# Performance work log

Hardware: AMD Instinct MI355X
Metric: run time of the kernel (lower is better)

Reference implementation:

```python
import jax, jax.numpy as jnp
import numpy as np

B, N, K = 8, 2048, 16
C_IN, HID, C_OUT = 128, 128, 128
MSG_DIM = 2 * C_IN + 3


def setup_inputs() -> dict:
    key = jax.random.key(0)
    ks = jax.random.split(key, 9)
    h = jax.random.normal(ks[0], (B, N, C_IN), dtype=jnp.float32)
    pos = jax.random.normal(ks[1], (B, N, 3), dtype=jnp.float32)
    idx = jax.random.randint(ks[2], (B, N, K), 0, N, dtype=jnp.int64)
    # MLP params (Linear: y = x @ W.T + b; store as (in, out) for einsum-free matmul)
    s1 = 1.0 / np.sqrt(MSG_DIM)
    s2 = 1.0 / np.sqrt(HID)
    W1 = jax.random.uniform(ks[3], (MSG_DIM, HID), minval=-s1, maxval=s1, dtype=jnp.float32)
    b1 = jax.random.uniform(ks[4], (HID,), minval=-s1, maxval=s1, dtype=jnp.float32)
    W2 = jax.random.uniform(ks[5], (HID, C_OUT), minval=-s2, maxval=s2, dtype=jnp.float32)
    b2 = jax.random.uniform(ks[6], (C_OUT,), minval=-s2, maxval=s2, dtype=jnp.float32)
    gamma = jnp.ones((C_OUT,), dtype=jnp.float32)
    beta = jnp.zeros((C_OUT,), dtype=jnp.float32)
    return {"h": h, "pos": pos, "idx": idx, "W1": W1, "b1": b1,
            "W2": W2, "b2": b2, "gamma": gamma, "beta": beta}


def _gather(feats, idx):
    # feats: (B,N,C), idx: (B,N,k) -> (B,N,k,C)
    return jax.vmap(lambda f, i: f[i])(feats, idx)


def _layernorm(x, gamma, beta, eps=1e-5):
    mu = jnp.mean(x, axis=-1, keepdims=True)
    var = jnp.mean(jnp.square(x - mu), axis=-1, keepdims=True)
    return (x - mu) * jax.lax.rsqrt(var + eps) * gamma + beta


def reference(h, pos, idx, W1, b1, W2, b2, gamma, beta):
    # h: (B,N,C), pos: (B,N,3), idx: (B,N,k)
    h_j = _gather(h, idx)                      # (B,N,k,C)
    rel = _gather(pos, idx) - pos[:, :, None]  # (B,N,k,3)
    h_i = jnp.broadcast_to(h[:, :, None, :], h_j.shape)
    msg = jnp.concatenate([h_i, h_j - h_i, rel], axis=-1)   # (B,N,k,2C+3)
    x = jax.nn.gelu(msg @ W1 + b1, approximate=False)       # (B,N,k,H)
    x = jax.nn.gelu(x @ W2 + b2, approximate=False)         # (B,N,k,O)
    out = jnp.max(x, axis=2)                                 # (B,N,O)
    return _layernorm(out, gamma, beta)
```

## Files before the change

kernel.cpp:

```cpp
#include <hip/hip_runtime.h>
#include <math.h>

#define NPTS 2048
#define KNBR 16

typedef __attribute__((ext_vector_type(8))) short bf16x8;
typedef __attribute__((ext_vector_type(4))) float f32x4;
union U8 { bf16x8 v; unsigned u[4]; };

static __device__ __forceinline__ unsigned pk2(float lo, float hi) {
    unsigned r;
    asm("v_cvt_pk_bf16_f32 %0, %1, %2" : "=v"(r) : "v"(lo), "v"(hi));
    return r;
}

static __device__ __forceinline__ float gelu(float x) {
    float x2 = x * x;
    float u  = x * fmaf(x2, 0.044715f, 1.0f);
    float e  = __expf(u * -1.5957691216057308f);
    return x * __builtin_amdgcn_rcpf(1.0f + e);
}

#define HSTR 136
#define LDS_SHORTS (36864 + 16 * 16 * HSTR)

__global__ __launch_bounds__(1024, 4) void edgeconv_fused(
    const float* __restrict__ h, const float* __restrict__ pos,
    const int* __restrict__ idx,
    const float* __restrict__ W1, const float* __restrict__ W2,
    const float* __restrict__ b1, const float* __restrict__ b2,
    const float* __restrict__ gamma, const float* __restrict__ beta,
    float* __restrict__ out)
{
    extern __shared__ short lds[];
    const int tid = threadIdx.x, wave = tid >> 6, lane = tid & 63;
    const int quad = lane >> 4, lm = lane & 15;

    for (int c = tid; c < 6656; c += 1024) {
        const int l = c & 63, fi = c >> 6;
        const int lrow = (l >> 4) * 8, lcol = l & 15;
        U8 t;
        if (fi < 40) {
            int ks = fi % 5, nt = fi / 5;
            int row0 = 128 + ks * 32 + lrow, col = nt * 16 + lcol;
            #pragma unroll
            for (int p = 0; p < 4; ++p) {
                int r0 = row0 + 2 * p;
                float v0 = (r0     < 259) ? W1[r0 * 128 + col]       : 0.f;
                float v1 = (r0 + 1 < 259) ? W1[(r0 + 1) * 128 + col] : 0.f;
                t.u[p] = pk2(v0, v1);
            }
        } else if (fi < 72) {
            int f2 = fi - 40, ks = f2 & 3, nt = f2 >> 2;
            int row0 = ks * 32 + lrow, col = nt * 16 + lcol;
            #pragma unroll
            for (int p = 0; p < 4; ++p)
                t.u[p] = pk2(W2[(row0 + 2*p) * 128 + col],
                             W2[(row0 + 2*p + 1) * 128 + col]);
        } else {
            int f2 = fi - 72, ks = f2 & 3, nt = f2 >> 2;
            int row0 = ks * 32 + lrow, col = nt * 16 + lcol;
            #pragma unroll
            for (int p = 0; p < 4; ++p)
                t.u[p] = pk2(W1[(row0 + 2*p) * 128 + col],
                             W1[(row0 + 2*p + 1) * 128 + col]);
        }
        ((bf16x8*)lds)[c] = t.v;
    }

    float b1v[8], b2v[8];
    #pragma unroll
    for (int nt = 0; nt < 8; ++nt) {
        b1v[nt] = b1[nt * 16 + lm];
        b2v[nt] = b2[nt * 16 + lm];
    }
    const float gv0 = gamma[(quad * 2) * 16 + lm];
    const float gv1 = gamma[(quad * 2 + 1) * 16 + lm];
    const float be0 = beta[(quad * 2) * 16 + lm];
    const float be1 = beta[(quad * 2 + 1) * 16 + lm];

    __syncthreads();

    const bf16x8* w1frag  = (const bf16x8*)lds;
    const bf16x8* w2frag  = (const bf16x8*)lds + 2560;
    const bf16x8* w1afrag = (const bf16x8*)lds + 4608;
    short* hrow = lds + 36864 + wave * 16 * HSTR;

    const int sb = (blockIdx.x & 7) * 32 + (blockIdx.x >> 3);
    const int node0 = sb * 64 + wave * 4;

    f32x4 basev[8];
    #pragma unroll
    for (int nt = 0; nt < 8; ++nt)
        basev[nt] = (f32x4){b1v[nt], b1v[nt], b1v[nt], b1v[nt]};
    {
        const float4* hsrc = (const float4*)h + (size_t)(node0 + (lm & 3)) * 32;
        bf16x8 af[4];
        #pragma unroll
        for (int ks = 0; ks < 4; ++ks) {
            float4 p0 = hsrc[ks * 8 + quad * 2];
            float4 p1 = hsrc[ks * 8 + quad * 2 + 1];
            U8 t;
            t.u[0] = pk2(p0.x, p0.y); t.u[1] = pk2(p0.z, p0.w);
            t.u[2] = pk2(p1.x, p1.y); t.u[3] = pk2(p1.z, p1.w);
            af[ks] = t.v;
        }
        #pragma unroll
        for (int ks = 0; ks < 4; ++ks)
            #pragma unroll
            for (int nt = 0; nt < 8; ++nt)
                basev[nt] = __builtin_amdgcn_mfma_f32_16x16x32_bf16(
                    af[ks], w1afrag[(nt * 4 + ks) * 64 + lane], basev[nt], 0, 0, 0);
    }
    __syncthreads();

    #pragma unroll
    for (int ni = 0; ni < 4; ++ni) {
        const int node = node0 + ni;
        const int b = node >> 11, n = node & 2047;
        const float4* hb4 = (const float4*)h + (size_t)b * NPTS * 32;
        const float*  pb  = pos + (size_t)b * NPTS * 3;

        const int jm = idx[node * KNBR + lm];

        bf16x8 afrag[4];
        #pragma unroll
        for (int ks = 0; ks < 4; ++ks) {
            float4 a0 = hb4[n  * 32 + ks * 8 + quad * 2];
            float4 a1 = hb4[n  * 32 + ks * 8 + quad * 2 + 1];
            float4 j0 = hb4[jm * 32 + ks * 8 + quad * 2];
            float4 j1 = hb4[jm * 32 + ks * 8 + quad * 2 + 1];
            U8 t;
            t.u[0] = pk2(j0.x - a0.x, j0.y - a0.y);
            t.u[1] = pk2(j0.z - a0.z, j0.w - a0.w);
            t.u[2] = pk2(j1.x - a1.x, j1.y - a1.y);
            t.u[3] = pk2(j1.z - a1.z, j1.w - a1.w);
            afrag[ks] = t.v;
        }
        U8 rt; rt.u[0] = 0; rt.u[1] = 0; rt.u[2] = 0; rt.u[3] = 0;
        if (quad == 0) {
            float rx = pb[3 * jm]     - pb[3 * n];
            float ry = pb[3 * jm + 1] - pb[3 * n + 1];
            float rz = pb[3 * jm + 2] - pb[3 * n + 2];
            rt.u[0] = pk2(rx, ry);
            rt.u[1] = pk2(rz, 0.0f);
        }

        f32x4 acc[8];
        #pragma unroll
        for (int nt = 0; nt < 8; ++nt) {
            float bv = basev[nt][ni];
            acc[nt] = (f32x4){bv, bv, bv, bv};
        }
        #pragma unroll
        for (int ks = 0; ks < 4; ++ks)
            #pragma unroll
            for (int nt = 0; nt < 8; ++nt)
                acc[nt] = __builtin_amdgcn_mfma_f32_16x16x32_bf16(
                    afrag[ks], w1frag[(nt * 5 + ks) * 64 + lane], acc[nt], 0, 0, 0);
        #pragma unroll
        for (int nt = 0; nt < 8; ++nt)
            acc[nt] = __builtin_amdgcn_mfma_f32_16x16x32_bf16(
                rt.v, w1frag[(nt * 5 + 4) * 64 + lane], acc[nt], 0, 0, 0);

        #pragma unroll
        for (int nt = 0; nt < 8; ++nt)
            #pragma unroll
            for (int r = 0; r < 4; ++r) {
                float g = gelu(acc[nt][r]);
                hrow[(quad * 4 + r) * HSTR + nt * 16 + lm] = (short)pk2(g, g);
            }
        asm volatile("s_waitcnt lgkmcnt(0)" ::: "memory");

        bf16x8 a2[4];
        #pragma unroll
        for (int ks = 0; ks < 4; ++ks)
            a2[ks] = *(const bf16x8*)(hrow + lm * HSTR + ks * 32 + quad * 8);

        f32x4 acc2[8];
        #pragma unroll
        for (int nt = 0; nt < 8; ++nt) acc2[nt] = (f32x4){0.f, 0.f, 0.f, 0.f};
        #pragma unroll
        for (int ks = 0; ks < 4; ++ks)
            #pragma unroll
            for (int nt = 0; nt < 8; ++nt)
                acc2[nt] = __builtin_amdgcn_mfma_f32_16x16x32_bf16(
                    a2[ks], w2frag[(nt * 4 + ks) * 64 + lane], acc2[nt], 0, 0, 0);

        float v[8];
        #pragma unroll
        for (int nt = 0; nt < 8; ++nt) {
            float mx = fmaxf(fmaxf(acc2[nt][0], acc2[nt][1]),
                             fmaxf(acc2[nt][2], acc2[nt][3]));
            float mn = fminf(fminf(acc2[nt][0], acc2[nt][1]),
                             fminf(acc2[nt][2], acc2[nt][3]));
            mx = fmaxf(mx, __shfl_xor(mx, 16, 64));
            mx = fmaxf(mx, __shfl_xor(mx, 32, 64));
            mn = fminf(mn, __shfl_xor(mn, 16, 64));
            mn = fminf(mn, __shfl_xor(mn, 32, 64));
            mx += b2v[nt]; mn += b2v[nt];
            v[nt] = fmaxf(gelu(mx), gelu(mn));
        }

        float s = 0.f, s2 = 0.f;
        #pragma unroll
        for (int nt = 0; nt < 8; ++nt) { s += v[nt]; s2 += v[nt] * v[nt]; }
        #pragma unroll
        for (int off = 1; off <= 8; off <<= 1) {
            s  += __shfl_xor(s,  off, 64);
            s2 += __shfl_xor(s2, off, 64);
        }
        const float mu  = s * (1.0f / 128.0f);
        const float var = s2 * (1.0f / 128.0f) - mu * mu;
        const float inv = rsqrtf(var + 1e-5f);

        float* orow = out + (size_t)node * 128;
        orow[(quad * 2) * 16 + lm]     = (v[quad * 2]     - mu) * inv * gv0 + be0;
        orow[(quad * 2 + 1) * 16 + lm] = (v[quad * 2 + 1] - mu) * inv * gv1 + be1;
    }
}

extern "C" void kernel_launch(void* const* d_in, const int* in_sizes, int n_in,
                              void* d_out, int out_size, void* d_ws, size_t ws_size,
                              hipStream_t stream) {
    const float* h     = (const float*)d_in[0];
    const float* pos   = (const float*)d_in[1];
    const int*   idx   = (const int*)  d_in[2];
    const float* W1    = (const float*)d_in[3];
    const float* b1    = (const float*)d_in[4];
    const float* W2    = (const float*)d_in[5];
    const float* b2    = (const float*)d_in[6];
    const float* gamma = (const float*)d_in[7];
    const float* beta  = (const float*)d_in[8];
    float* out = (float*)d_out;

    hipFuncSetAttribute((const void*)edgeconv_fused,
                        hipFuncAttributeMaxDynamicSharedMemorySize,
                        LDS_SHORTS * 2);
    edgeconv_fused<<<256, 1024, LDS_SHORTS * 2, stream>>>(
        h, pos, idx, W1, W2, b1, b2, gamma, beta, out);
}
```

Measured before the change: 122.4 us.

## Process node pairs with prefetched neighbor gathers and chunked GELU staging

Each wave now handles two nodes at a time, sharing each W1/W2 fragment LDS load across two MFMA chains. Neighbor feature and position gathers for the next pair are issued early into registers so global latency overlaps compute. The per-node first-layer base is written to LDS instead of kept in registers, and the GELU staging buffer is cut to 32-column chunks. This raises register pressure and adds extra LDS waits per chunk, and LDS grows to 144 KB.

```diff
diff --git a/kernel.cpp b/kernel.cpp
--- a/kernel.cpp
+++ b/kernel.cpp
@@ -1,5 +1,4 @@
 #include <hip/hip_runtime.h>
-#include <math.h>
 
 #define NPTS 2048
 #define KNBR 16
@@ -21,8 +20,8 @@
     return x * __builtin_amdgcn_rcpf(1.0f + e);
 }
 
-#define HSTR 136
-#define LDS_SHORTS (36864 + 16 * 16 * HSTR)
+#define STG 40
+#define LDS_BYTES 147456
 
 __global__ __launch_bounds__(1024, 4) void edgeconv_fused(
     const float* __restrict__ h, const float* __restrict__ pos,
@@ -33,6 +32,7 @@
     float* __restrict__ out)
 {
     extern __shared__ short lds[];
+    float* ldsF = (float*)lds;
     const int tid = threadIdx.x, wave = tid >> 6, lane = tid & 63;
     const int quad = lane >> 4, lm = lane & 15;
 
@@ -84,17 +84,26 @@
     const bf16x8* w1frag  = (const bf16x8*)lds;
     const bf16x8* w2frag  = (const bf16x8*)lds + 2560;
     const bf16x8* w1afrag = (const bf16x8*)lds + 4608;
-    short* hrow = lds + 36864 + wave * 16 * HSTR;
+    short* stg   = lds  + 36864 + wave * 1280;
+    float* baseF = ldsF + 28672 + wave * 512;
 
     const int sb = (blockIdx.x & 7) * 32 + (blockIdx.x >> 3);
     const int node0 = sb * 64 + wave * 4;
-
-    f32x4 basev[8];
+    const int bidx = node0 >> 11;
+    const float4* hb4 = (const float4*)h + (size_t)bidx * NPTS * 32;
+    const float*  pb  = pos + (size_t)bidx * NPTS * 3;
+    const int nloc = node0 & 2047;
+
+    int idxv[4];
     #pragma unroll
-    for (int nt = 0; nt < 8; ++nt)
-        basev[nt] = (f32x4){b1v[nt], b1v[nt], b1v[nt], b1v[nt]};
+    for (int ni = 0; ni < 4; ++ni)
+        idxv[ni] = idx[(node0 + ni) * KNBR + lm];
+
+    float4 hjA[8], hjB[8];
+    float pjxA, pjyA, pjzA, pjxB, pjyB, pjzB;
+
     {
-        const float4* hsrc = (const float4*)h + (size_t)(node0 + (lm & 3)) * 32;
+        const float4* hsrc = hb4 + (size_t)(nloc + (lm & 3)) * 32;
         bf16x8 af[4];
         #pragma unroll
         for (int ks = 0; ks < 4; ++ks) {
@@ -105,118 +114,173 @@
             t.u[2] = pk2(p1.x, p1.y); t.u[3] = pk2(p1.z, p1.w);
             af[ks] = t.v;
         }
+        f32x4 bacc[8];
+        #pragma unroll
+        for (int nt = 0; nt < 8; ++nt)
+            bacc[nt] = (f32x4){b1v[nt], b1v[nt], b1v[nt], b1v[nt]};
         #pragma unroll
         for (int ks = 0; ks < 4; ++ks)
             #pragma unroll
             for (int nt = 0; nt < 8; ++nt)
-                basev[nt] = __builtin_amdgcn_mfma_f32_16x16x32_bf16(
-                    af[ks], w1afrag[(nt * 4 + ks) * 64 + lane], basev[nt], 0, 0, 0);
+                bacc[nt] = __builtin_amdgcn_mfma_f32_16x16x32_bf16(
+                    af[ks], w1afrag[(nt * 4 + ks) * 64 + lane], bacc[nt], 0, 0, 0);
+
+        {
+            const float4* ja = hb4 + (size_t)idxv[0] * 32;
+            const float4* jb = hb4 + (size_t)idxv[1] * 32;
+            #pragma unroll
+            for (int ks = 0; ks < 4; ++ks) {
+                hjA[2*ks]   = ja[ks * 8 + quad * 2];
+                hjA[2*ks+1] = ja[ks * 8 + quad * 2 + 1];
+                hjB[2*ks]   = jb[ks * 8 + quad * 2];
+                hjB[2*ks+1] = jb[ks * 8 + quad * 2 + 1];
+            }
+            pjxA = pb[3*idxv[0]]; pjyA = pb[3*idxv[0]+1]; pjzA = pb[3*idxv[0]+2];
+            pjxB = pb[3*idxv[1]]; pjyB = pb[3*idxv[1]+1]; pjzB = pb[3*idxv[1]+2];
+        }
+
+        if (quad == 0)
+            #pragma unroll
+            for (int nt = 0; nt < 8; ++nt)
+                #pragma unroll
+                for (int r = 0; r < 4; ++r)
+                    baseF[r * 128 + nt * 16 + lm] = bacc[nt][r];
     }
     __syncthreads();
 
     #pragma unroll
-    for (int ni = 0; ni < 4; ++ni) {
-        const int node = node0 + ni;
-        const int b = node >> 11, n = node & 2047;
-        const float4* hb4 = (const float4*)h + (size_t)b * NPTS * 32;
-        const float*  pb  = pos + (size_t)b * NPTS * 3;
-
-        const int jm = idx[node * KNBR + lm];
-
-        bf16x8 afrag[4];
-        #pragma unroll
-        for (int ks = 0; ks < 4; ++ks) {
-            float4 a0 = hb4[n  * 32 + ks * 8 + quad * 2];
-            float4 a1 = hb4[n  * 32 + ks * 8 + quad * 2 + 1];
-            float4 j0 = hb4[jm * 32 + ks * 8 + quad * 2];
-            float4 j1 = hb4[jm * 32 + ks * 8 + quad * 2 + 1];
-            U8 t;
-            t.u[0] = pk2(j0.x - a0.x, j0.y - a0.y);
-            t.u[1] = pk2(j0.z - a0.z, j0.w - a0.w);
-            t.u[2] = pk2(j1.x - a1.x, j1.y - a1.y);
-            t.u[3] = pk2(j1.z - a1.z, j1.w - a1.w);
-            afrag[ks] = t.v;
-        }
-        U8 rt; rt.u[0] = 0; rt.u[1] = 0; rt.u[2] = 0; rt.u[3] = 0;
-        if (quad == 0) {
-            float rx = pb[3 * jm]     - pb[3 * n];
-            float ry = pb[3 * jm + 1] - pb[3 * n + 1];
-            float rz = pb[3 * jm + 2] - pb[3 * n + 2];
-            rt.u[0] = pk2(rx, ry);
-            rt.u[1] = pk2(rz, 0.0f);
-        }
-
-        f32x4 acc[8];
+    for (int pr = 0; pr < 2; ++pr) {
+        const int na = pr * 2, nb = pr * 2 + 1;
+
+        bf16x8 afA[4], afB[4];
+        U8 rlA, rlB;
+        {
+            const float4* hiA4 = hb4 + (size_t)(nloc + na) * 32;
+            const float4* hiB4 = hb4 + (size_t)(nloc + nb) * 32;
+            #pragma unroll
+            for (int ks = 0; ks < 4; ++ks) {
+                float4 a0 = hiA4[ks * 8 + quad * 2];
+                float4 a1 = hiA4[ks * 8 + quad * 2 + 1];
+                float4 b0 = hiB4[ks * 8 + quad * 2];
+                float4 b1_ = hiB4[ks * 8 + quad * 2 + 1];
+                float4 j0 = hjA[2*ks], j1 = hjA[2*ks+1];
+                float4 k0 = hjB[2*ks], k1 = hjB[2*ks+1];
+                U8 t;
+                t.u[0] = pk2(j0.x - a0.x, j0.y - a0.y);
+                t.u[1] = pk2(j0.z - a0.z, j0.w - a0.w);
+                t.u[2] = pk2(j1.x - a1.x, j1.y - a1.y);
+                t.u[3] = pk2(j1.z - a1.z, j1.w - a1.w);
+                afA[ks] = t.v;
+                t.u[0] = pk2(k0.x - b0.x, k0.y - b0.y);
+                t.u[1] = pk2(k0.z - b0.z, k0.w - b0.w);
+                t.u[2] = pk2(k1.x - b1_.x, k1.y - b1_.y);
+                t.u[3] = pk2(k1.z - b1_.z, k1.w - b1_.w);
+                afB[ks] = t.v;
+            }
+            rlA.u[0] = 0; rlA.u[1] = 0; rlA.u[2] = 0; rlA.u[3] = 0;
+            rlB.u[0] = 0; rlB.u[1] = 0; rlB.u[2] = 0; rlB.u[3] = 0;
+            if (quad == 0) {
+                int ia = nloc + na, ib = nloc + nb;
+                rlA.u[0] = pk2(pjxA - pb[3*ia], pjyA - pb[3*ia+1]);
+                rlA.u[1] = pk2(pjzA - pb[3*ia+2], 0.f);
+                rlB.u[0] = pk2(pjxB - pb[3*ib], pjyB - pb[3*ib+1]);
+                rlB.u[1] = pk2(pjzB - pb[3*ib+2], 0.f);
+            }
+        }
+
+        bf16x8 a2A[4], a2B[4];
+        #pragma unroll
+        for (int ks2 = 0; ks2 < 4; ++ks2) {
+            #pragma unroll
+            for (int ntl = 0; ntl < 2; ++ntl) {
+                const int nt = ks2 * 2 + ntl;
+                float bA = baseF[na * 128 + nt * 16 + lm];
+                float bB = baseF[nb * 128 + nt * 16 + lm];
+                f32x4 cA = (f32x4){bA, bA, bA, bA};
+                f32x4 cB = (f32x4){bB, bB, bB, bB};
+                #pragma unroll
+                for (int ks = 0; ks < 4; ++ks) {
+                    bf16x8 w = w1frag[(nt * 5 + ks) * 64 + lane];
+                    cA = __builtin_amdgcn_mfma_f32_16x16x32_bf16(afA[ks], w, cA, 0, 0, 0);
+                    cB = __builtin_amdgcn_mfma_f32_16x16x32_bf16(afB[ks], w, cB, 0, 0, 0);
+                }
+                {
+                    bf16x8 w = w1frag[(nt * 5 + 4) * 64 + lane];
+                    cA = __builtin_amdgcn_mfma_f32_16x16x32_bf16(rlA.v, w, cA, 0, 0, 0);
+                    cB = __builtin_amdgcn_mfma_f32_16x16x32_bf16(rlB.v, w, cB, 0, 0, 0);
+                }
+                #pragma unroll
+                for (int r = 0; r < 4; ++r) {
+                    float gA = gelu(cA[r]), gB = gelu(cB[r]);
+                    stg[      (quad * 4 + r) * STG + ntl * 16 + lm] = (short)pk2(gA, gA);
+                    stg[640 + (quad * 4 + r) * STG + ntl * 16 + lm] = (short)pk2(gB, gB);
+                }
+            }
+            asm volatile("s_waitcnt lgkmcnt(0)" ::: "memory");
+            a2A[ks2] = *(const bf16x8*)(stg +       lm * STG + quad * 8);
+            a2B[ks2] = *(const bf16x8*)(stg + 640 + lm * STG + quad * 8);
+            asm volatile("s_waitcnt lgkmcnt(0)" ::: "memory");
+        }
+
+        if (pr == 0) {
+            const float4* ja = hb4 + (size_t)idxv[2] * 32;
+            const float4* jb = hb4 + (size_t)idxv[3] * 32;
+            #pragma unroll
+            for (int ks = 0; ks < 4; ++ks) {
+                hjA[2*ks]   = ja[ks * 8 + quad * 2];
+                hjA[2*ks+1] = ja[ks * 8 + quad * 2 + 1];
+                hjB[2*ks]   = jb[ks * 8 + quad * 2];
+                hjB[2*ks+1] = jb[ks * 8 + quad * 2 + 1];
+            }
+            pjxA = pb[3*idxv[2]]; pjyA = pb[3*idxv[2]+1]; pjzA = pb[3*idxv[2]+2];
+            pjxB = pb[3*idxv[3]]; pjyB = pb[3*idxv[3]+1]; pjzB = pb[3*idxv[3]+2];
+        }
+
+        float vA[8], vB[8];
         #pragma unroll
         for (int nt = 0; nt < 8; ++nt) {
-            float bv = basev[nt][ni];
-            acc[nt] = (f32x4){bv, bv, bv, bv};
-        }
-        #pragma unroll
-        for (int ks = 0; ks < 4; ++ks)
-            #pragma unroll
-            for (int nt = 0; nt < 8; ++nt)
-                acc[nt] = __builtin_amdgcn_mfma_f32_16x16x32_bf16(
-                    afrag[ks], w1frag[(nt * 5 + ks) * 64 + lane], acc[nt], 0, 0, 0);
-        #pragma unroll
-        for (int nt = 0; nt < 8; ++nt)
-            acc[nt] = __builtin_amdgcn_mfma_f32_16x16x32_bf16(
-                rt.v, w1frag[(nt * 5 + 4) * 64 + lane], acc[nt], 0, 0, 0);
-
-        #pragma unroll
-        for (int nt = 0; nt < 8; ++nt)
-            #pragma unroll
-            for (int r = 0; r < 4; ++r) {
-                float g = gelu(acc[nt][r]);
-                hrow[(quad * 4 + r) * HSTR + nt * 16 + lm] = (short)pk2(g, g);
-            }
-        asm volatile("s_waitcnt lgkmcnt(0)" ::: "memory");
-
-        bf16x8 a2[4];
-        #pragma unroll
-        for (int ks = 0; ks < 4; ++ks)
-            a2[ks] = *(const bf16x8*)(hrow + lm * HSTR + ks * 32 + quad * 8);
-
-        f32x4 acc2[8];
-        #pragma unroll
-        for (int nt = 0; nt < 8; ++nt) acc2[nt] = (f32x4){0.f, 0.f, 0.f, 0.f};
-        #pragma unroll
-        for (int ks = 0; ks < 4; ++ks)
-            #pragma unroll
-            for (int nt = 0; nt < 8; ++nt)
-                acc2[nt] = __builtin_amdgcn_mfma_f32_16x16x32_bf16(
-                    a2[ks], w2frag[(nt * 4 + ks) * 64 + lane], acc2[nt], 0, 0, 0);
-
-        float v[8];
-        #pragma unroll
-        for (int nt = 0; nt < 8; ++nt) {
-            float mx = fmaxf(fmaxf(acc2[nt][0], acc2[nt][1]),
-                             fmaxf(acc2[nt][2], acc2[nt][3]));
-            float mn = fminf(fminf(acc2[nt][0], acc2[nt][1]),
-                             fminf(acc2[nt][2], acc2[nt][3]));
-            mx = fmaxf(mx, __shfl_xor(mx, 16, 64));
-            mx = fmaxf(mx, __shfl_xor(mx, 32, 64));
-            mn = fminf(mn, __shfl_xor(mn, 16, 64));
-            mn = fminf(mn, __shfl_xor(mn, 32, 64));
-            mx += b2v[nt]; mn += b2v[nt];
-            v[nt] = fmaxf(gelu(mx), gelu(mn));
-        }
-
-        float s = 0.f, s2 = 0.f;
-        #pragma unroll
-        for (int nt = 0; nt < 8; ++nt) { s += v[nt]; s2 += v[nt] * v[nt]; }
-        #pragma unroll
-        for (int off = 1; off <= 8; off <<= 1) {
-            s  += __shfl_xor(s,  off, 64);
-            s2 += __shfl_xor(s2, off, 64);
-        }
-        const float mu  = s * (1.0f / 128.0f);
-        const float var = s2 * (1.0f / 128.0f) - mu * mu;
-        const float inv = rsqrtf(var + 1e-5f);
-
-        float* orow = out + (size_t)node * 128;
-        orow[(quad * 2) * 16 + lm]     = (v[quad * 2]     - mu) * inv * gv0 + be0;
-        orow[(quad * 2 + 1) * 16 + lm] = (v[quad * 2 + 1] - mu) * inv * gv1 + be1;
+            f32x4 cA = (f32x4){0.f, 0.f, 0.f, 0.f};
+            f32x4 cB = (f32x4){0.f, 0.f, 0.f, 0.f};
+            #pragma unroll
+            for (int ks = 0; ks < 4; ++ks) {
+                bf16x8 w = w2frag[(nt * 4 + ks) * 64 + lane];
+                cA = __builtin_amdgcn_mfma_f32_16x16x32_bf16(a2A[ks], w, cA, 0, 0, 0);
+                cB = __builtin_amdgcn_mfma_f32_16x16x32_bf16(a2B[ks], w, cB, 0, 0, 0);
+            }
+            float mxA = fmaxf(fmaxf(cA[0], cA[1]), fmaxf(cA[2], cA[3]));
+            float mnA = fminf(fminf(cA[0], cA[1]), fminf(cA[2], cA[3]));
+            float mxB = fmaxf(fmaxf(cB[0], cB[1]), fmaxf(cB[2], cB[3]));
+            float mnB = fminf(fminf(cB[0], cB[1]), fminf(cB[2], cB[3]));
+            mxA = fmaxf(mxA, __shfl_xor(mxA, 16, 64));
+            mxA = fmaxf(mxA, __shfl_xor(mxA, 32, 64));
+            mnA = fminf(mnA, __shfl_xor(mnA, 16, 64));
+            mnA = fminf(mnA, __shfl_xor(mnA, 32, 64));
+            mxB = fmaxf(mxB, __shfl_xor(mxB, 16, 64));
+            mxB = fmaxf(mxB, __shfl_xor(mxB, 32, 64));
+            mnB = fminf(mnB, __shfl_xor(mnB, 16, 64));
+            mnB = fminf(mnB, __shfl_xor(mnB, 32, 64));
+            vA[nt] = fmaxf(gelu(mxA + b2v[nt]), gelu(mnA + b2v[nt]));
+            vB[nt] = fmaxf(gelu(mxB + b2v[nt]), gelu(mnB + b2v[nt]));
+        }
+
+        #pragma unroll
+        for (int u = 0; u < 2; ++u) {
+            const float* v = u ? vB : vA;
+            float s = 0.f, s2 = 0.f;
+            #pragma unroll
+            for (int nt = 0; nt < 8; ++nt) { s += v[nt]; s2 += v[nt] * v[nt]; }
+            #pragma unroll
+            for (int off = 1; off <= 8; off <<= 1) {
+                s  += __shfl_xor(s,  off, 64);
+                s2 += __shfl_xor(s2, off, 64);
+            }
+            const float mu  = s * (1.0f / 128.0f);
+            const float var = s2 * (1.0f / 128.0f) - mu * mu;
+            const float inv = rsqrtf(var + 1e-5f);
+            float* orow = out + (size_t)(node0 + pr * 2 + u) * 128;
+            orow[(quad * 2) * 16 + lm]     = (v[quad * 2]     - mu) * inv * gv0 + be0;
+            orow[(quad * 2 + 1) * 16 + lm] = (v[quad * 2 + 1] - mu) * inv * gv1 + be1;
+        }
     }
 }
 
@@ -235,8 +299,7 @@
     float* out = (float*)d_out;
 
     hipFuncSetAttribute((const void*)edgeconv_fused,
-                        hipFuncAttributeMaxDynamicSharedMemorySize,
-                        LDS_SHORTS * 2);
-    edgeconv_fused<<<256, 1024, LDS_SHORTS * 2, stream>>>(
+                        hipFuncAttributeMaxDynamicSharedMemorySize, LDS_BYTES);
+    edgeconv_fused<<<256, 1024, LDS_BYTES, stream>>>(
         h, pos, idx, W1, W2, b1, b2, gamma, beta, out);
 }
```

After: 123.4 us. No clear change (+0.8%).

## Precompute per-node W1 projection and gather projected features instead of raw h

Applied to the files above, without the earlier changes.

The first linear layer is split algebraically: h_i@(W1a-W1b) plus b1 is computed once per center node, and h_j@W1b is precomputed for every node by a new first kernel into a bf16 workspace. The edge kernel then gathers these 128-wide bf16 rows, adds the relative-position term with scalar FMAs, and applies GELU. This removes the per-edge first-layer MFMAs and the LDS round-trip for the hidden activations. The cost is an extra kernel launch, a global write and re-read of the projected table, and bf16 rounding of the precomputed projection. It also prefetches the next node's gathered rows and switches GELU to exp2.

```diff
diff --git a/kernel.cpp b/kernel.cpp
--- a/kernel.cpp
+++ b/kernel.cpp
@@ -1,5 +1,4 @@
 #include <hip/hip_runtime.h>
-#include <math.h>
 
 #define NPTS 2048
 #define KNBR 16
@@ -7,6 +6,7 @@
 typedef __attribute__((ext_vector_type(8))) short bf16x8;
 typedef __attribute__((ext_vector_type(4))) float f32x4;
 union U8 { bf16x8 v; unsigned u[4]; };
+union F4 { f32x4 v; float4 q; };
 
 static __device__ __forceinline__ unsigned pk2(float lo, float hi) {
     unsigned r;
@@ -17,63 +17,116 @@
 static __device__ __forceinline__ float gelu(float x) {
     float x2 = x * x;
     float u  = x * fmaf(x2, 0.044715f, 1.0f);
-    float e  = __expf(u * -1.5957691216057308f);
+    float e  = __builtin_amdgcn_exp2f(u * -2.3022083f);
     return x * __builtin_amdgcn_rcpf(1.0f + e);
 }
 
-#define HSTR 136
-#define LDS_SHORTS (36864 + 16 * 16 * HSTR)
-
-__global__ __launch_bounds__(1024, 4) void edgeconv_fused(
+__global__ __launch_bounds__(1024) void edge_phase1(
+    const float* __restrict__ h, const float* __restrict__ W1,
+    short* __restrict__ G)
+{
+    __shared__ short w1bfs[16384];
+    const int tid = threadIdx.x, lane = tid & 63, wave = tid >> 6;
+    const int quad = lane >> 4, lm = lane & 15;
+
+    for (int c = tid; c < 2048; c += 1024) {
+        const int l = c & 63, fi = c >> 6;
+        const int lrow = (l >> 4) * 8, lcol = l & 15;
+        const int ks = fi & 3, nt = fi >> 2;
+        const int row0 = 128 + ks * 32 + lrow, col = nt * 16 + lcol;
+        U8 t;
+        #pragma unroll
+        for (int p = 0; p < 4; ++p)
+            t.u[p] = pk2(W1[(row0 + 2*p) * 128 + col],
+                         W1[(row0 + 2*p + 1) * 128 + col]);
+        ((bf16x8*)w1bfs)[c] = t.v;
+    }
+    __syncthreads();
+    const bf16x8* w1bf = (const bf16x8*)w1bfs;
+
+    const int sb = (blockIdx.x & 7) * 32 + (blockIdx.x >> 3);
+    const int node0 = sb * 64 + wave * 4;
+    const int bidx = node0 >> 11, nloc = node0 & 2047;
+    const float4* hb4 = (const float4*)h + (size_t)bidx * NPTS * 32;
+    short* Gb = G + (size_t)bidx * NPTS * 128;
+
+    const float4* hsrc = hb4 + (size_t)(nloc + (lm & 3)) * 32;
+    bf16x8 af[4];
+    #pragma unroll
+    for (int ks = 0; ks < 4; ++ks) {
+        float4 p0 = hsrc[ks * 8 + quad * 2];
+        float4 p1 = hsrc[ks * 8 + quad * 2 + 1];
+        U8 t;
+        t.u[0] = pk2(p0.x, p0.y); t.u[1] = pk2(p0.z, p0.w);
+        t.u[2] = pk2(p1.x, p1.y); t.u[3] = pk2(p1.z, p1.w);
+        af[ks] = t.v;
+    }
+    f32x4 gacc[8];
+    #pragma unroll
+    for (int nt = 0; nt < 8; ++nt) gacc[nt] = (f32x4){0.f, 0.f, 0.f, 0.f};
+    #pragma unroll
+    for (int ks = 0; ks < 4; ++ks)
+        #pragma unroll
+        for (int nt = 0; nt < 8; ++nt)
+            gacc[nt] = __builtin_amdgcn_mfma_f32_16x16x32_bf16(
+                w1bf[(nt * 4 + ks) * 64 + lane], af[ks], gacc[nt], 0, 0, 0);
+
+    if (lm < 4)
+        #pragma unroll
+        for (int nt = 0; nt < 8; ++nt) {
+            uint2 gw;
+            gw.x = pk2(gacc[nt][0], gacc[nt][1]);
+            gw.y = pk2(gacc[nt][2], gacc[nt][3]);
+            *(uint2*)(Gb + (size_t)(nloc + lm) * 128 + nt * 16 + quad * 4) = gw;
+        }
+}
+
+#define LDS2_BYTES 99840
+
+__global__ __launch_bounds__(1024, 4) void edge_phase2(
     const float* __restrict__ h, const float* __restrict__ pos,
     const int* __restrict__ idx,
     const float* __restrict__ W1, const float* __restrict__ W2,
     const float* __restrict__ b1, const float* __restrict__ b2,
     const float* __restrict__ gamma, const float* __restrict__ beta,
+    const short* __restrict__ G,
     float* __restrict__ out)
 {
     extern __shared__ short lds[];
+    float* ldsF = (float*)lds;
     const int tid = threadIdx.x, wave = tid >> 6, lane = tid & 63;
     const int quad = lane >> 4, lm = lane & 15;
 
-    for (int c = tid; c < 6656; c += 1024) {
+    for (int c = tid; c < 4096; c += 1024) {
         const int l = c & 63, fi = c >> 6;
         const int lrow = (l >> 4) * 8, lcol = l & 15;
         U8 t;
-        if (fi < 40) {
-            int ks = fi % 5, nt = fi / 5;
-            int row0 = 128 + ks * 32 + lrow, col = nt * 16 + lcol;
-            #pragma unroll
-            for (int p = 0; p < 4; ++p) {
-                int r0 = row0 + 2 * p;
-                float v0 = (r0     < 259) ? W1[r0 * 128 + col]       : 0.f;
-                float v1 = (r0 + 1 < 259) ? W1[(r0 + 1) * 128 + col] : 0.f;
-                t.u[p] = pk2(v0, v1);
-            }
-        } else if (fi < 72) {
-            int f2 = fi - 40, ks = f2 & 3, nt = f2 >> 2;
+        if (fi < 32) {
+            int ks = fi & 3, nt = fi >> 2;
             int row0 = ks * 32 + lrow, col = nt * 16 + lcol;
             #pragma unroll
             for (int p = 0; p < 4; ++p)
                 t.u[p] = pk2(W2[(row0 + 2*p) * 128 + col],
                              W2[(row0 + 2*p + 1) * 128 + col]);
         } else {
-            int f2 = fi - 72, ks = f2 & 3, nt = f2 >> 2;
+            int f2 = fi - 32, ks = f2 & 3, nt = f2 >> 2;
             int row0 = ks * 32 + lrow, col = nt * 16 + lcol;
             #pragma unroll
-            for (int p = 0; p < 4; ++p)
-                t.u[p] = pk2(W1[(row0 + 2*p) * 128 + col],
-                             W1[(row0 + 2*p + 1) * 128 + col]);
+            for (int p = 0; p < 4; ++p) {
+                int r0 = row0 + 2 * p;
+                float v0 = W1[r0 * 128 + col]       - W1[(r0 + 128) * 128 + col];
+                float v1 = W1[(r0 + 1) * 128 + col] - W1[(r0 + 129) * 128 + col];
+                t.u[p] = pk2(v0, v1);
+            }
         }
         ((bf16x8*)lds)[c] = t.v;
     }
-
-    float b1v[8], b2v[8];
-    #pragma unroll
-    for (int nt = 0; nt < 8; ++nt) {
-        b1v[nt] = b1[nt * 16 + lm];
-        b2v[nt] = b2[nt * 16 + lm];
-    }
+    if (tid < 384)
+        ldsF[16384 + tid] = W1[(256 + (tid >> 7)) * 128 + (tid & 127)];
+
+    float b2v[8];
+    #pragma unroll
+    for (int nt = 0; nt < 8; ++nt) b2v[nt] = b2[nt * 16 + lm];
     const float gv0 = gamma[(quad * 2) * 16 + lm];
     const float gv1 = gamma[(quad * 2 + 1) * 16 + lm];
     const float be0 = beta[(quad * 2) * 16 + lm];
@@ -81,20 +134,30 @@
 
     __syncthreads();
 
-    const bf16x8* w1frag  = (const bf16x8*)lds;
-    const bf16x8* w2frag  = (const bf16x8*)lds + 2560;
-    const bf16x8* w1afrag = (const bf16x8*)lds + 4608;
-    short* hrow = lds + 36864 + wave * 16 * HSTR;
+    const bf16x8* w2frag = (const bf16x8*)lds;
+    const bf16x8* w1df   = (const bf16x8*)lds + 2048;
+    const float*  w1rL   = ldsF + 16384;
+    float* baseW = ldsF + 16768 + wave * 512;
 
     const int sb = (blockIdx.x & 7) * 32 + (blockIdx.x >> 3);
     const int node0 = sb * 64 + wave * 4;
-
-    f32x4 basev[8];
-    #pragma unroll
-    for (int nt = 0; nt < 8; ++nt)
-        basev[nt] = (f32x4){b1v[nt], b1v[nt], b1v[nt], b1v[nt]};
+    const int bidx = node0 >> 11, nloc = node0 & 2047;
+    const float4* hb4 = (const float4*)h + (size_t)bidx * NPTS * 32;
+    const float*  pb  = pos + (size_t)bidx * NPTS * 3;
+    const short*  Gb  = G + (size_t)bidx * NPTS * 128;
+
+    int idxv[4];
+    #pragma unroll
+    for (int ni = 0; ni < 4; ++ni)
+        idxv[ni] = idx[(node0 + ni) * KNBR + lm];
+
+    bf16x8 gcur[4], gnxt[4];
+    #pragma unroll
+    for (int ks = 0; ks < 4; ++ks)
+        gcur[ks] = *(const bf16x8*)(Gb + (size_t)idxv[0] * 128 + ks * 32 + quad * 8);
+
     {
-        const float4* hsrc = (const float4*)h + (size_t)(node0 + (lm & 3)) * 32;
+        const float4* hsrc = hb4 + (size_t)(nloc + (lm & 3)) * 32;
         bf16x8 af[4];
         #pragma unroll
         for (int ks = 0; ks < 4; ++ks) {
@@ -105,106 +168,95 @@
             t.u[2] = pk2(p1.x, p1.y); t.u[3] = pk2(p1.z, p1.w);
             af[ks] = t.v;
         }
+        f32x4 bacc[8];
+        #pragma unroll
+        for (int nt = 0; nt < 8; ++nt) {
+            F4 bi; bi.q = *(const float4*)(b1 + nt * 16 + quad * 4);
+            bacc[nt] = bi.v;
+        }
         #pragma unroll
         for (int ks = 0; ks < 4; ++ks)
             #pragma unroll
             for (int nt = 0; nt < 8; ++nt)
-                basev[nt] = __builtin_amdgcn_mfma_f32_16x16x32_bf16(
-                    af[ks], w1afrag[(nt * 4 + ks) * 64 + lane], basev[nt], 0, 0, 0);
-    }
-    __syncthreads();
+                bacc[nt] = __builtin_amdgcn_mfma_f32_16x16x32_bf16(
+                    w1df[(nt * 4 + ks) * 64 + lane], af[ks], bacc[nt], 0, 0, 0);
+        if (lm < 4)
+            #pragma unroll
+            for (int nt = 0; nt < 8; ++nt) {
+                F4 o; o.v = bacc[nt];
+                *(float4*)(baseW + lm * 128 + nt * 16 + quad * 4) = o.q;
+            }
+    }
 
     #pragma unroll
     for (int ni = 0; ni < 4; ++ni) {
-        const int node = node0 + ni;
-        const int b = node >> 11, n = node & 2047;
-        const float4* hb4 = (const float4*)h + (size_t)b * NPTS * 32;
-        const float*  pb  = pos + (size_t)b * NPTS * 3;
-
-        const int jm = idx[node * KNBR + lm];
-
-        bf16x8 afrag[4];
+        const int j = idxv[ni], i = nloc + ni;
+        const float rx = pb[3*j]   - pb[3*i];
+        const float ry = pb[3*j+1] - pb[3*i+1];
+        const float rz = pb[3*j+2] - pb[3*i+2];
+
+        bf16x8 a2[4];
         #pragma unroll
         for (int ks = 0; ks < 4; ++ks) {
-            float4 a0 = hb4[n  * 32 + ks * 8 + quad * 2];
-            float4 a1 = hb4[n  * 32 + ks * 8 + quad * 2 + 1];
-            float4 j0 = hb4[jm * 32 + ks * 8 + quad * 2];
-            float4 j1 = hb4[jm * 32 + ks * 8 + quad * 2 + 1];
+            U8 g; g.v = gcur[ks];
+            float gf[8];
+            #pragma unroll
+            for (int p = 0; p < 4; ++p) {
+                gf[2*p]   = __builtin_bit_cast(float, g.u[p] << 16);
+                gf[2*p+1] = __builtin_bit_cast(float, g.u[p] & 0xffff0000u);
+            }
+            const int ko = ks * 32 + quad * 8;
+            F4 bl0, bl1, w00, w01, w10, w11, w20, w21;
+            bl0.q = *(const float4*)(baseW + ni * 128 + ko);
+            bl1.q = *(const float4*)(baseW + ni * 128 + ko + 4);
+            w00.q = *(const float4*)(w1rL + ko);       w01.q = *(const float4*)(w1rL + ko + 4);
+            w10.q = *(const float4*)(w1rL + 128 + ko); w11.q = *(const float4*)(w1rL + 128 + ko + 4);
+            w20.q = *(const float4*)(w1rL + 256 + ko); w21.q = *(const float4*)(w1rL + 256 + ko + 4);
+            float gl[8];
+            #pragma unroll
+            for (int e = 0; e < 8; ++e) {
+                float bb = (e < 4) ? bl0.v[e] : bl1.v[e-4];
+                float w0 = (e < 4) ? w00.v[e] : w01.v[e-4];
+                float w1v= (e < 4) ? w10.v[e] : w11.v[e-4];
+                float w2v= (e < 4) ? w20.v[e] : w21.v[e-4];
+                float hp = gf[e] + bb;
+                hp = fmaf(rx, w0, hp);
+                hp = fmaf(ry, w1v, hp);
+                hp = fmaf(rz, w2v, hp);
+                gl[e] = gelu(hp);
+            }
             U8 t;
-            t.u[0] = pk2(j0.x - a0.x, j0.y - a0.y);
-            t.u[1] = pk2(j0.z - a0.z, j0.w - a0.w);
-            t.u[2] = pk2(j1.x - a1.x, j1.y - a1.y);
-            t.u[3] = pk2(j1.z - a1.z, j1.w - a1.w);
-            afrag[ks] = t.v;
-        }
-        U8 rt; rt.u[0] = 0; rt.u[1] = 0; rt.u[2] = 0; rt.u[3] = 0;
-        if (quad == 0) {
-            float rx = pb[3 * jm]     - pb[3 * n];
-            float ry = pb[3 * jm + 1] - pb[3 * n + 1];
-            float rz = pb[3 * jm + 2] - pb[3 * n + 2];
-            rt.u[0] = pk2(rx, ry);
-            rt.u[1] = pk2(rz, 0.0f);
-        }
-
-        f32x4 acc[8];
+            t.u[0] = pk2(gl[0], gl[1]); t.u[1] = pk2(gl[2], gl[3]);
+            t.u[2] = pk2(gl[4], gl[5]); t.u[3] = pk2(gl[6], gl[7]);
+            a2[ks] = t.v;
+        }
+
+        if (ni < 3) {
+            #pragma unroll
+            for (int ks = 0; ks < 4; ++ks)
+                gnxt[ks] = *(const bf16x8*)(Gb + (size_t)idxv[ni+1] * 128 + ks * 32 + quad * 8);
+        }
+
+        float vA[8];
         #pragma unroll
         for (int nt = 0; nt < 8; ++nt) {
-            float bv = basev[nt][ni];
-            acc[nt] = (f32x4){bv, bv, bv, bv};
-        }
-        #pragma unroll
-        for (int ks = 0; ks < 4; ++ks)
-            #pragma unroll
-            for (int nt = 0; nt < 8; ++nt)
-                acc[nt] = __builtin_amdgcn_mfma_f32_16x16x32_bf16(
-                    afrag[ks], w1frag[(nt * 5 + ks) * 64 + lane], acc[nt], 0, 0, 0);
-        #pragma unroll
-        for (int nt = 0; nt < 8; ++nt)
-            acc[nt] = __builtin_amdgcn_mfma_f32_16x16x32_bf16(
-                rt.v, w1frag[(nt * 5 + 4) * 64 + lane], acc[nt], 0, 0, 0);
-
-        #pragma unroll
-        for (int nt = 0; nt < 8; ++nt)
-            #pragma unroll
-            for (int r = 0; r < 4; ++r) {
-                float g = gelu(acc[nt][r]);
-                hrow[(quad * 4 + r) * HSTR + nt * 16 + lm] = (short)pk2(g, g);
-            }
-        asm volatile("s_waitcnt lgkmcnt(0)" ::: "memory");
-
-        bf16x8 a2[4];
-        #pragma unroll
-        for (int ks = 0; ks < 4; ++ks)
-            a2[ks] = *(const bf16x8*)(hrow + lm * HSTR + ks * 32 + quad * 8);
-
-        f32x4 acc2[8];
-        #pragma unroll
-        for (int nt = 0; nt < 8; ++nt) acc2[nt] = (f32x4){0.f, 0.f, 0.f, 0.f};
-        #pragma unroll
-        for (int ks = 0; ks < 4; ++ks)
-            #pragma unroll
-            for (int nt = 0; nt < 8; ++nt)
-                acc2[nt] = __builtin_amdgcn_mfma_f32_16x16x32_bf16(
-                    a2[ks], w2frag[(nt * 4 + ks) * 64 + lane], acc2[nt], 0, 0, 0);
-
-        float v[8];
-        #pragma unroll
-        for (int nt = 0; nt < 8; ++nt) {
-            float mx = fmaxf(fmaxf(acc2[nt][0], acc2[nt][1]),
-                             fmaxf(acc2[nt][2], acc2[nt][3]));
-            float mn = fminf(fminf(acc2[nt][0], acc2[nt][1]),
-                             fminf(acc2[nt][2], acc2[nt][3]));
+            f32x4 cA = (f32x4){0.f, 0.f, 0.f, 0.f};
+            #pragma unroll
+            for (int ks = 0; ks < 4; ++ks)
+                cA = __builtin_amdgcn_mfma_f32_16x16x32_bf16(
+                    a2[ks], w2frag[(nt * 4 + ks) * 64 + lane], cA, 0, 0, 0);
+            float mx = fmaxf(fmaxf(cA[0], cA[1]), fmaxf(cA[2], cA[3]));
+            float mn = fminf(fminf(cA[0], cA[1]), fminf(cA[2], cA[3]));
             mx = fmaxf(mx, __shfl_xor(mx, 16, 64));
             mx = fmaxf(mx, __shfl_xor(mx, 32, 64));
             mn = fminf(mn, __shfl_xor(mn, 16, 64));
             mn = fminf(mn, __shfl_xor(mn, 32, 64));
-            mx += b2v[nt]; mn += b2v[nt];
-            v[nt] = fmaxf(gelu(mx), gelu(mn));
+            vA[nt] = fmaxf(gelu(mx + b2v[nt]), gelu(mn + b2v[nt]));
         }
 
         float s = 0.f, s2 = 0.f;
         #pragma unroll
-        for (int nt = 0; nt < 8; ++nt) { s += v[nt]; s2 += v[nt] * v[nt]; }
+        for (int nt = 0; nt < 8; ++nt) { s += vA[nt]; s2 += vA[nt] * vA[nt]; }
         #pragma unroll
         for (int off = 1; off <= 8; off <<= 1) {
             s  += __shfl_xor(s,  off, 64);
@@ -213,10 +265,12 @@
         const float mu  = s * (1.0f / 128.0f);
         const float var = s2 * (1.0f / 128.0f) - mu * mu;
         const float inv = rsqrtf(var + 1e-5f);
-
-        float* orow = out + (size_t)node * 128;
-        orow[(quad * 2) * 16 + lm]     = (v[quad * 2]     - mu) * inv * gv0 + be0;
-        orow[(quad * 2 + 1) * 16 + lm] = (v[quad * 2 + 1] - mu) * inv * gv1 + be1;
+        float* orow = out + (size_t)(node0 + ni) * 128;
+        orow[(quad * 2) * 16 + lm]     = (vA[quad * 2]     - mu) * inv * gv0 + be0;
+        orow[(quad * 2 + 1) * 16 + lm] = (vA[quad * 2 + 1] - mu) * inv * gv1 + be1;
+
+        #pragma unroll
+        for (int ks = 0; ks < 4; ++ks) gcur[ks] = gnxt[ks];
     }
 }
 
@@ -234,9 +288,12 @@
     const float* beta  = (const float*)d_in[8];
     float* out = (float*)d_out;
 
-    hipFuncSetAttribute((const void*)edgeconv_fused,
-                        hipFuncAttributeMaxDynamicSharedMemorySize,
-                        LDS_SHORTS * 2);
-    edgeconv_fused<<<256, 1024, LDS_SHORTS * 2, stream>>>(
-        h, pos, idx, W1, W2, b1, b2, gamma, beta, out);
-}
+    short* G = (short*)d_ws;
+
+    edge_phase1<<<256, 1024, 0, stream>>>(h, W1, G);
+
+    hipFuncSetAttribute((const void*)edge_phase2,
+                        hipFuncAttributeMaxDynamicSharedMemorySize, LDS2_BYTES);
+    edge_phase2<<<256, 1024, LDS2_BYTES, stream>>>(
+        h, pos, idx, W1, W2, b1, b2, gamma, beta, G, out);
+}
```

Measured after the change: 174.7 us. +42.8%, slower.
